# Optimization experiments

Hardware: AMD Instinct MI355X
Metric: run time of the kernel (lower is better)

Reference implementation:

```python
import jax, jax.numpy as jnp
import numpy as np

N = 50000   # nodes per side
H = 256     # hidden_dim
E = 800000  # edges per metapath (avg degree 16)
XAVIER_STD = 0.088  # gain 1.414 * sqrt(2/(H+H))


def setup_inputs() -> dict:
    key = jax.random.key(0)
    ks = jax.random.split(key, 32)
    inp = {}
    inp["h_d"] = jax.random.normal(ks[0], (N, H), dtype=jnp.float32)
    inp["h_p"] = jax.random.normal(ks[1], (N, H), dtype=jnp.float32)
    i = 2
    for name in ["d0", "d1", "p0", "p1"]:
        inp[name + "_idx"] = jax.random.randint(ks[i], (2, E), 0, N, dtype=jnp.int32); i += 1
        inp[name + "_val"] = jax.random.uniform(ks[i], (E,), dtype=jnp.float32); i += 1
    # per-metapath GCN params: Linear weight [H,H] (no bias), additive bias [H], PReLU slope (scalar)
    for name in ["d0", "d1", "p0", "p1"]:
        inp["W" + name] = jax.random.normal(ks[i], (H, H), dtype=jnp.float32) * XAVIER_STD; i += 1
        inp["b" + name] = jnp.zeros((H,), jnp.float32)
        inp["a" + name] = jnp.full((1,), 0.25, jnp.float32)
    # per-side attention params: fc weight/bias, att vector [1,H]
    for s in ["d", "p"]:
        inp["fcW" + s] = jax.random.normal(ks[i], (H, H), dtype=jnp.float32) * XAVIER_STD; i += 1
        inp["fcb" + s] = jnp.zeros((H,), jnp.float32)
        inp["att" + s] = jax.random.normal(ks[i], (1, H), dtype=jnp.float32) * XAVIER_STD; i += 1
    return inp


def _gcn(h, W, b, a, idx, val):
    # Linear (no bias) -> sparse COO spmm -> bias -> PReLU
    fts = h @ W.T                                  # [N,H]
    msg = val[:, None] * fts[idx[1]]               # gather source rows [E,H]
    out = jax.ops.segment_sum(msg, idx[0], num_segments=h.shape[0]) + b
    return jnp.where(out > 0, out, a * out)        # PReLU, shared slope


def _attn_fuse(embeds, Wf, bf, att):
    # score_p = att . mean_n(tanh(fc(embed_p)))  -> softmax over metapaths
    sp = jnp.stack([jnp.tanh(e @ Wf.T + bf).mean(axis=0) for e in embeds])  # [P,H]
    beta = jax.nn.softmax(sp @ att[0])                                      # [P]
    return jnp.einsum('p,pnh->nh', beta, jnp.stack(embeds))


def reference(h_d, h_p, d0_idx, d0_val, d1_idx, d1_val, p0_idx, p0_val,
              p1_idx, p1_val, Wd0, bd0, ad0, Wd1, bd1, ad1,
              Wp0, bp0, ap0, Wp1, bp1, ap1,
              fcWd, fcbd, attd, fcWp, fcbp, attp):
    embeds_d = [_gcn(h_d, Wd0, bd0, ad0, d0_idx, d0_val),
                _gcn(h_d, Wd1, bd1, ad1, d1_idx, d1_val)]
    z_d = _attn_fuse(embeds_d, fcWd, fcbd, attd)
    embeds_p = [_gcn(h_p, Wp0, bp0, ap0, p0_idx, p0_val),
                _gcn(h_p, Wp1, bp1, ap1, p1_idx, p1_val)]
    z_p = _attn_fuse(embeds_p, fcWp, fcbp, attp)
    return (z_d, z_p)
```

## Files before the change

kernel.cpp:

```cpp
#include <hip/hip_runtime.h>
#include <cstdint>

#define H 256
#define NBMAX 400
#define CAPB 16

typedef unsigned short u16;
typedef __attribute__((ext_vector_type(8))) short short8;
typedef __attribute__((ext_vector_type(4))) float f32x4;

__device__ __forceinline__ float bf2f(u16 u) {
  return __uint_as_float(((unsigned)u) << 16);
}
__device__ __forceinline__ u16 f2bf(float f) {
  unsigned u = __float_as_uint(f);
  u = (u + 0x7FFF + ((u >> 16) & 1)) >> 16;
  return (u16)u;
}
__device__ __forceinline__ void async16(const void* g, void* l) {
  __builtin_amdgcn_global_load_lds((const __attribute__((address_space(1))) void*)g,
                                   (__attribute__((address_space(3))) void*)l, 16, 0, 0);
}

__global__ __launch_bounds__(256) void cvt_bf16(
    const float* __restrict__ src, u16* __restrict__ dst, int total)
{
  int i = (blockIdx.x * 256 + threadIdx.x) * 4;
  if (i >= total) return;
  float4 x = *(const float4*)(src + i);
  *(ushort4*)(dst + i) = make_ushort4(f2bf(x.x), f2bf(x.y), f2bf(x.z), f2bf(x.w));
}

__global__ __launch_bounds__(256) void cvt_weights(
    const float* w0, const float* w1, const float* w2, const float* w3,
    const float* w4, const float* w5, u16* __restrict__ dst)
{
  const float* srcs[6] = {w0, w1, w2, w3, w4, w5};
  const float* s = srcs[blockIdx.y];
  int i = (blockIdx.x * 256 + threadIdx.x) * 4;
  float4 x = *(const float4*)(s + i);
  *(ushort4*)(dst + blockIdx.y * (H * H) + i) =
      make_ushort4(f2bf(x.x), f2bf(x.y), f2bf(x.z), f2bf(x.w));
}

__device__ __forceinline__ int block_incl_scan(int v) {
  __shared__ int wsum[4];
  int tid = threadIdx.x, lane = tid & 63, w = tid >> 6;
  int x = v;
  #pragma unroll
  for (int off = 1; off < 64; off <<= 1) {
    int n = __shfl_up(x, off);
    if (lane >= off) x += n;
  }
  if (lane == 63) wsum[w] = x;
  __syncthreads();
  int add = 0;
  #pragma unroll
  for (int i = 0; i < 4; ++i) add += (i < w) ? wsum[i] : 0;
  return x + add;
}

__global__ __launch_bounds__(1024) void hist_coarse(
    const int* i0, const int* i1, const int* i2, const int* i3,
    int* __restrict__ bcnt, int E, int nbuck)
{
  int mp = blockIdx.y;
  const int* idxs[4] = {i0, i1, i2, i3};
  const int* idx = idxs[mp];
  __shared__ int lh[NBMAX];
  int t = threadIdx.x;
  for (int i = t; i < nbuck; i += 1024) lh[i] = 0;
  __syncthreads();
  for (int e = blockIdx.x * 1024 + t; e < E; e += gridDim.x * 1024)
    atomicAdd(&lh[idx[e] >> 7], 1);
  __syncthreads();
  for (int i = t; i < nbuck; i += 1024) {
    int v = lh[i];
    if (v) atomicAdd(&bcnt[mp * nbuck + i], v);
  }
}

__global__ __launch_bounds__(256) void scan_buckets(
    const int* __restrict__ bcnt, int* __restrict__ bbase,
    int* __restrict__ gcur, int* __restrict__ rowptr, int N, int E, int nbuck)
{
  int mp = blockIdx.y;
  int t = threadIdx.x;
  int i0 = t * 2, i1 = t * 2 + 1;
  int a = (i0 < nbuck) ? bcnt[mp * nbuck + i0] : 0;
  int b = (i1 < nbuck) ? bcnt[mp * nbuck + i1] : 0;
  int s = a + b;
  int incl = block_incl_scan(s);
  int ex = incl - s;
  if (i0 < nbuck) { bbase[mp * nbuck + i0] = ex;     gcur[mp * nbuck + i0] = ex; }
  if (i1 < nbuck) { bbase[mp * nbuck + i1] = ex + a; gcur[mp * nbuck + i1] = ex + a; }
  if (t == 0) rowptr[mp * (N + 1) + N] = E;
}

__global__ __launch_bounds__(1024) void scatter_binned(
    const int* i0, const int* i1, const int* i2, const int* i3,
    const float* v0, const float* v1, const float* v2, const float* v3,
    int* __restrict__ gcur, int2* __restrict__ edgesB, int E, int nbuck)
{
  int mp = blockIdx.y;
  const int* idxs[4] = {i0, i1, i2, i3};
  const float* vals[4] = {v0, v1, v2, v3};
  const int* idx = idxs[mp];
  const float* val = vals[mp];
  int* cur = gcur + mp * nbuck;
  int2* out = edgesB + (size_t)mp * E;

  __shared__ int cnt[NBMAX];
  __shared__ int2 slab[NBMAX * CAPB];
  int t = threadIdx.x;
  for (int i = t; i < nbuck; i += 1024) cnt[i] = 0;
  __syncthreads();

  for (int base_e = blockIdx.x * 2048; base_e < E; base_e += gridDim.x * 2048) {
    #pragma unroll
    for (int u = 0; u < 2; ++u) {
      int e = base_e + u * 1024 + t;
      if (e < E) {
        int d = idx[e];
        int s = idx[E + e];
        float v = val[e];
        int bb = d >> 7;
        int2 pk = make_int2(s | ((d & 127) << 16), __float_as_int(v));
        int slot = atomicAdd(&cnt[bb], 1);
        if (slot < CAPB) slab[bb * CAPB + slot] = pk;
        else {
          int pos = atomicAdd(&cur[bb], 1);
          out[pos] = pk;
        }
      }
    }
    __syncthreads();
    for (int bb = t; bb < nbuck; bb += 1024) {
      int c = cnt[bb];
      if (c > CAPB) c = CAPB;
      if (c >= 8) {
        int ng = c >> 3;
        int pos = atomicAdd(&cur[bb], ng * 8);
        for (int k = 0; k < ng * 8; ++k) out[pos + k] = slab[bb * CAPB + k];
        int r = c & 7;
        for (int k = 0; k < r; ++k)
          slab[bb * CAPB + k] = slab[bb * CAPB + ng * 8 + k];
        cnt[bb] = r;
      }
    }
    __syncthreads();
  }
  for (int bb = t; bb < nbuck; bb += 1024) {
    int c = cnt[bb];
    if (c > CAPB) c = CAPB;
    if (c > 0) {
      int pos = atomicAdd(&cur[bb], c);
      for (int k = 0; k < c; ++k) out[pos + k] = slab[bb * CAPB + k];
    }
  }
}

__global__ __launch_bounds__(256) void bucket_to_csr(
    const int2* __restrict__ edgesB, const int* __restrict__ bbase,
    int* __restrict__ rowptr, int2* __restrict__ edges, int N, int E, int nbuck)
{
  int mp = blockIdx.y;
  int b = blockIdx.x;
  int base = bbase[mp * nbuck + b];
  int endp = (b + 1 < nbuck) ? bbase[mp * nbuck + b + 1] : E;
  int cntE = endp - base;
  const int2* in = edgesB + (size_t)mp * E + base;
  int2* out = edges + (size_t)mp * E;

  __shared__ int h[128], csum[128];
  int t = threadIdx.x;
  if (t < 128) h[t] = 0;
  __syncthreads();
  for (int k = t; k < cntE; k += 256)
    atomicAdd(&h[(in[k].x >> 16) & 127], 1);
  __syncthreads();
  if (t == 0) {
    int acc = 0;
    for (int i = 0; i < 128; ++i) { int c = h[i]; csum[i] = acc; acc += c; }
  }
  __syncthreads();
  int d0 = b << 7;
  if (t < 128 && d0 + t < N) rowptr[mp * (N + 1) + d0 + t] = base + csum[t];
  if (t < 128) h[t] = csum[t];
  __syncthreads();
  for (int k = t; k < cntE; k += 256) {
    int2 pk = in[k];
    int dl = (pk.x >> 16) & 127;
    int pos = atomicAdd(&h[dl], 1);
    out[base + pos] = make_int2(pk.x & 0xFFFF, pk.y);
  }
}

__global__ __launch_bounds__(256) void spmm_csr(
    const u16* __restrict__ fts, const int* __restrict__ rowptr,
    const int2* __restrict__ edges, const float* __restrict__ bias,
    const float* __restrict__ alpha, u16* __restrict__ e, int N)
{
  int gw = (int)((blockIdx.x * 256 + threadIdx.x) >> 6);
  if (gw >= N) return;
  int lane = threadIdx.x & 63;
  int beg = rowptr[gw], end = rowptr[gw + 1];
  float a0 = 0.f, a1 = 0.f, a2 = 0.f, a3 = 0.f;
  for (int base = beg; base < end; base += 64) {
    int k = base + lane;
    int2 ev = make_int2(0, 0);
    if (k < end) ev = edges[k];
    int cnt = min(64, end - base);
    int j = 0;
    for (; j + 4 <= cnt; j += 4) {
      int sj[4]; float vj[4]; ushort4 r[4];
      #pragma unroll
      for (int u = 0; u < 4; ++u) {
        sj[u] = __shfl(ev.x, j + u);
        vj[u] = __uint_as_float((unsigned)__shfl(ev.y, j + u));
      }
      #pragma unroll
      for (int u = 0; u < 4; ++u)
        r[u] = *(const ushort4*)(fts + (size_t)sj[u] * H + lane * 4);
      #pragma unroll
      for (int u = 0; u < 4; ++u) {
        a0 += vj[u] * bf2f(r[u].x);
        a1 += vj[u] * bf2f(r[u].y);
        a2 += vj[u] * bf2f(r[u].z);
        a3 += vj[u] * bf2f(r[u].w);
      }
    }
    for (; j < cnt; ++j) {
      int sj = __shfl(ev.x, j);
      float vj = __uint_as_float((unsigned)__shfl(ev.y, j));
      ushort4 r = *(const ushort4*)(fts + (size_t)sj * H + lane * 4);
      a0 += vj * bf2f(r.x);
      a1 += vj * bf2f(r.y);
      a2 += vj * bf2f(r.z);
      a3 += vj * bf2f(r.w);
    }
  }
  int c = lane * 4;
  float al = alpha[0];
  float r0 = a0 + bias[c],     r1 = a1 + bias[c + 1];
  float r2 = a2 + bias[c + 2], r3 = a3 + bias[c + 3];
  r0 = r0 > 0.f ? r0 : al * r0;
  r1 = r1 > 0.f ? r1 : al * r1;
  r2 = r2 > 0.f ? r2 : al * r2;
  r3 = r3 > 0.f ? r3 : al * r3;
  *(ushort4*)(e + (size_t)gw * H + c) =
      make_ushort4(f2bf(r0), f2bf(r1), f2bf(r2), f2bf(r3));
}

template <int MODE>
__global__ __launch_bounds__(256) void gemm_bt(
    const u16* __restrict__ A, const u16* __restrict__ W,
    u16* __restrict__ C, const float* __restrict__ bias,
    float* __restrict__ colsum, int M)
{
  __shared__ u16 As[128 * 64];
  __shared__ u16 Bs[128 * 64];
  const int tid  = threadIdx.x;
  const int lane = tid & 63;
  const int wave = tid >> 6;
  const int quad = lane >> 4;
  const int l15  = lane & 15;
  const int m0 = blockIdx.x * 128;
  const int n0 = blockIdx.y * 128;
  const int wr = (wave & 1) * 64;
  const int wc = (wave >> 1) * 64;

  f32x4 acc[4][4] = {};

  for (int k0 = 0; k0 < H; k0 += 64) {
    #pragma unroll
    for (int r = 0; r < 4; ++r) {
      int chunk = r * 256 + tid;
      int row = chunk >> 3;
      int col = (chunk & 7) * 8;
      int gm = m0 + row; if (gm >= M) gm = M - 1;
      u16* lbase = As + (r * 256 + wave * 64) * 8;
      async16(A + gm * H + k0 + col, lbase);
      u16* lbase2 = Bs + (r * 256 + wave * 64) * 8;
      async16(W + (n0 + row) * H + k0 + col, lbase2);
    }
    __syncthreads();
    #pragma unroll
    for (int kk = 0; kk < 64; kk += 32) {
      short8 af[4], bf[4];
      #pragma unroll
      for (int i = 0; i < 4; ++i) {
        af[i] = *(const short8*)(As + (wr + i * 16 + l15) * 64 + kk + quad * 8);
        bf[i] = *(const short8*)(Bs + (wc + i * 16 + l15) * 64 + kk + quad * 8);
      }
      #pragma unroll
      for (int mi = 0; mi < 4; ++mi)
        #pragma unroll
        for (int ni = 0; ni < 4; ++ni)
          acc[mi][ni] = __builtin_amdgcn_mfma_f32_16x16x32_bf16(af[mi], bf[ni], acc[mi][ni], 0, 0, 0);
    }
    __syncthreads();
  }

  if (MODE == 0) {
    #pragma unroll
    for (int mi = 0; mi < 4; ++mi)
      #pragma unroll
      for (int ni = 0; ni < 4; ++ni) {
        int n = n0 + wc + ni * 16 + l15;
        #pragma unroll
        for (int j = 0; j < 4; ++j) {
          int m = m0 + wr + mi * 16 + quad * 4 + j;
          if (m < M) C[m * H + n] = f2bf(acc[mi][ni][j]);
        }
      }
  } else {
    #pragma unroll
    for (int ni = 0; ni < 4; ++ni) {
      int n = n0 + wc + ni * 16 + l15;
      float bv = bias[n];
      float s = 0.f;
      #pragma unroll
      for (int mi = 0; mi < 4; ++mi)
        #pragma unroll
        for (int j = 0; j < 4; ++j) {
          int m = m0 + wr + mi * 16 + quad * 4 + j;
          if (m < M) {
            float x = acc[mi][ni][j] + bv;
            s += 1.f - 2.f / (__expf(2.f * x) + 1.f);
          }
        }
      s += __shfl_xor(s, 16);
      s += __shfl_xor(s, 32);
      if (lane < 16) unsafeAtomicAdd(&colsum[n], s);
    }
  }
}

__global__ __launch_bounds__(256) void compute_beta(
    const float* __restrict__ sp, const float* __restrict__ att,
    float invN, float* __restrict__ beta)
{
  __shared__ float red0[4], red1[4];
  int t = threadIdx.x;
  float a = att[t];
  float s0 = sp[t] * invN * a;
  float s1 = sp[H + t] * invN * a;
  #pragma unroll
  for (int off = 32; off > 0; off >>= 1) {
    s0 += __shfl_down(s0, off);
    s1 += __shfl_down(s1, off);
  }
  int lane = t & 63, w = t >> 6;
  if (lane == 0) { red0[w] = s0; red1[w] = s1; }
  __syncthreads();
  if (t == 0) {
    float a0 = red0[0] + red0[1] + red0[2] + red0[3];
    float a1 = red1[0] + red1[1] + red1[2] + red1[3];
    float mx = fmaxf(a0, a1);
    float e0v = __expf(a0 - mx), e1v = __expf(a1 - mx);
    float inv = 1.f / (e0v + e1v);
    beta[0] = e0v * inv;
    beta[1] = e1v * inv;
  }
}

__global__ __launch_bounds__(256) void fuse_out(
    const u16* __restrict__ e0, const u16* __restrict__ e1,
    const float* __restrict__ beta, float* __restrict__ out, int total)
{
  int i = (blockIdx.x * 256 + threadIdx.x) * 4;
  if (i >= total) return;
  float b0 = beta[0], b1 = beta[1];
  ushort4 u0 = *(const ushort4*)(e0 + i);
  ushort4 u1 = *(const ushort4*)(e1 + i);
  float4 o;
  o.x = b0 * bf2f(u0.x) + b1 * bf2f(u1.x);
  o.y = b0 * bf2f(u0.y) + b1 * bf2f(u1.y);
  o.z = b0 * bf2f(u0.z) + b1 * bf2f(u1.z);
  o.w = b0 * bf2f(u0.w) + b1 * bf2f(u1.w);
  *(float4*)(out + i) = o;
}

extern "C" void kernel_launch(void* const* d_in, const int* in_sizes, int n_in,
                              void* d_out, int out_size, void* d_ws, size_t ws_size,
                              hipStream_t stream)
{
  const float* h_in[2] = {(const float*)d_in[0], (const float*)d_in[1]};
  const int N = in_sizes[0] / H;
  const int E = in_sizes[3];
  const int* idx[4]; const float* val[4];
  for (int i = 0; i < 4; ++i) {
    idx[i] = (const int*)d_in[2 + 2 * i];
    val[i] = (const float*)d_in[3 + 2 * i];
  }
  const float *W[4], *bia[4], *alp[4];
  for (int i = 0; i < 4; ++i) {
    W[i]   = (const float*)d_in[10 + 3 * i];
    bia[i] = (const float*)d_in[11 + 3 * i];
    alp[i] = (const float*)d_in[12 + 3 * i];
  }
  const float *fcW[2], *fcb[2], *att[2];
  for (int s = 0; s < 2; ++s) {
    fcW[s] = (const float*)d_in[22 + 3 * s];
    fcb[s] = (const float*)d_in[23 + 3 * s];
    att[s] = (const float*)d_in[24 + 3 * s];
  }

  const size_t NH = (size_t)N * H;
  const int nbuck = (N + 127) >> 7;
  auto align256 = [](size_t x) { return (x + 255) & ~(size_t)255; };
  char* p = (char*)d_ws;
  u16* fts = (u16*)p;      p += align256(NH * 2);
  u16* e0b = (u16*)p;      p += align256(NH * 2);
  u16* hbf = (u16*)p;      p += align256(NH * 2);
  u16* Wbf = (u16*)p;      p += align256((size_t)6 * H * H * 2);
  int* bcnt = (int*)p;     p += align256((size_t)4 * NBMAX * 4);
  int* bbase = (int*)p;    p += align256((size_t)4 * NBMAX * 4);
  int* gcur = (int*)p;     p += align256((size_t)4 * NBMAX * 4);
  int* rowptr = (int*)p;   p += align256((size_t)4 * (N + 1) * 4);
  int2* edges = (int2*)p;  p += align256((size_t)4 * E * 8);
  float* sp = (float*)p;   p += align256((size_t)2 * H * 4);
  float* beta = (float*)p;
  u16* e1b = hbf;
  int2* edgesB = (int2*)fts;

  const int gx = (N + 127) / 128;
  dim3 ggrid(gx, 2);
  const int tot = (int)NH;
  const int el_blocks = tot / 4 / 256;
  const int spmm_blocks = (N + 3) / 4;

  dim3 wgrid(H * H / 1024, 6);
  cvt_weights<<<wgrid, 256, 0, stream>>>(W[0], W[1], W[2], W[3], fcW[0], fcW[1], Wbf);

  hipMemsetAsync(bcnt, 0, (size_t)4 * NBMAX * 4, stream);
  hist_coarse<<<dim3(64, 4), 1024, 0, stream>>>(idx[0], idx[1], idx[2], idx[3],
                                                bcnt, E, nbuck);
  scan_buckets<<<dim3(1, 4), 256, 0, stream>>>(bcnt, bbase, gcur, rowptr, N, E, nbuck);
  scatter_binned<<<dim3(64, 4), 1024, 0, stream>>>(idx[0], idx[1], idx[2], idx[3],
                                                   val[0], val[1], val[2], val[3],
                                                   gcur, edgesB, E, nbuck);
  bucket_to_csr<<<dim3(nbuck, 4), 256, 0, stream>>>(edgesB, bbase, rowptr, edges,
                                                    N, E, nbuck);

  for (int s = 0; s < 2; ++s) {
    float* outz = (float*)d_out + (size_t)s * NH;
    cvt_bf16<<<el_blocks, 256, 0, stream>>>(h_in[s], hbf, tot);

    for (int m = 0; m < 2; ++m) {
      int pi = s * 2 + m;
      gemm_bt<0><<<ggrid, 256, 0, stream>>>(hbf, Wbf + (size_t)pi * H * H, fts,
                                            nullptr, nullptr, N);
      spmm_csr<<<spmm_blocks, 256, 0, stream>>>(
          fts, rowptr + (size_t)pi * (N + 1), edges + (size_t)pi * E,
          bia[pi], alp[pi], m == 0 ? e0b : e1b, N);
    }
    hipMemsetAsync(sp, 0, 2 * H * 4, stream);
    gemm_bt<1><<<ggrid, 256, 0, stream>>>(e0b, Wbf + (size_t)(4 + s) * H * H,
                                          nullptr, fcb[s], sp, N);
    gemm_bt<1><<<ggrid, 256, 0, stream>>>(e1b, Wbf + (size_t)(4 + s) * H * H,
                                          nullptr, fcb[s], sp + H, N);
    compute_beta<<<1, 256, 0, stream>>>(sp, att[s], 1.0f / (float)N, beta);
    fuse_out<<<el_blocks, 256, 0, stream>>>(e0b, e1b, beta, outz, tot);
  }
}
```

Before: 808.4 us.

## Batch all four metapaths into single grid-dimension launches per stage

Replaces the per-side, per-metapath loop of many small launches with one launch per stage (convert, projection GEMM, SpMM, attention GEMM, beta, fuse), each indexing its metapath or side through an extra grid dimension. This cuts launch count and serialization gaps and gives each launch more blocks to fill the GPU. In exchange the workspace grows to hold all four feature and embedding buffers at once, which raises memory footprint and may reduce L2 reuse. Index arithmetic is widened to size_t to handle the larger buffers.

```diff
diff --git a/kernel.cpp b/kernel.cpp
--- a/kernel.cpp
+++ b/kernel.cpp
@@ -23,12 +23,15 @@
 }
 
 __global__ __launch_bounds__(256) void cvt_bf16(
-    const float* __restrict__ src, u16* __restrict__ dst, int total)
-{
+    const float* __restrict__ h0, const float* __restrict__ h1,
+    u16* __restrict__ dst, int total, size_t NH)
+{
+  const float* src = blockIdx.y ? h1 : h0;
+  u16* d = dst + (size_t)blockIdx.y * NH;
   int i = (blockIdx.x * 256 + threadIdx.x) * 4;
   if (i >= total) return;
   float4 x = *(const float4*)(src + i);
-  *(ushort4*)(dst + i) = make_ushort4(f2bf(x.x), f2bf(x.y), f2bf(x.z), f2bf(x.w));
+  *(ushort4*)(d + i) = make_ushort4(f2bf(x.x), f2bf(x.y), f2bf(x.z), f2bf(x.w));
 }
 
 __global__ __launch_bounds__(256) void cvt_weights(
@@ -197,10 +200,22 @@
 }
 
 __global__ __launch_bounds__(256) void spmm_csr(
-    const u16* __restrict__ fts, const int* __restrict__ rowptr,
-    const int2* __restrict__ edges, const float* __restrict__ bias,
-    const float* __restrict__ alpha, u16* __restrict__ e, int N)
-{
+    const u16* __restrict__ ftsAll, const int* __restrict__ rowptrAll,
+    const int2* __restrict__ edgesAll,
+    const float* b0, const float* b1, const float* b2, const float* b3,
+    const float* a0ptr, const float* a1ptr, const float* a2ptr, const float* a3ptr,
+    u16* __restrict__ eAll, int N, int E, size_t NH)
+{
+  int mp = blockIdx.y;
+  const u16* fts = ftsAll + (size_t)mp * NH;
+  const int* rowptr = rowptrAll + (size_t)mp * (N + 1);
+  const int2* edges = edgesAll + (size_t)mp * E;
+  const float* biases[4] = {b0, b1, b2, b3};
+  const float* alphas[4] = {a0ptr, a1ptr, a2ptr, a3ptr};
+  const float* bias = biases[mp];
+  const float* alpha = alphas[mp];
+  u16* e = eAll + (size_t)mp * NH;
+
   int gw = (int)((blockIdx.x * 256 + threadIdx.x) >> 6);
   if (gw >= N) return;
   int lane = threadIdx.x & 63;
@@ -254,10 +269,24 @@
 
 template <int MODE>
 __global__ __launch_bounds__(256) void gemm_bt(
-    const u16* __restrict__ A, const u16* __restrict__ W,
-    u16* __restrict__ C, const float* __restrict__ bias,
-    float* __restrict__ colsum, int M)
-{
+    const u16* __restrict__ Abase, const u16* __restrict__ Wbase,
+    u16* __restrict__ Cbase, const float* fcb0, const float* fcb1,
+    float* __restrict__ colsum, int M, size_t NH)
+{
+  const int pi = blockIdx.z;
+  const u16* A; const u16* W; u16* C = nullptr;
+  const float* bias = nullptr; float* cs = nullptr;
+  if (MODE == 0) {
+    A = Abase + (size_t)(pi >> 1) * NH;
+    W = Wbase + (size_t)pi * (H * H);
+    C = Cbase + (size_t)pi * NH;
+  } else {
+    A = Abase + (size_t)pi * NH;
+    W = Wbase + (size_t)(pi >> 1) * (H * H);
+    bias = (pi >> 1) ? fcb1 : fcb0;
+    cs = colsum + (size_t)pi * H;
+  }
+
   __shared__ u16 As[128 * 64];
   __shared__ u16 Bs[128 * 64];
   const int tid  = threadIdx.x;
@@ -280,9 +309,9 @@
       int col = (chunk & 7) * 8;
       int gm = m0 + row; if (gm >= M) gm = M - 1;
       u16* lbase = As + (r * 256 + wave * 64) * 8;
-      async16(A + gm * H + k0 + col, lbase);
+      async16(A + (size_t)gm * H + k0 + col, lbase);
       u16* lbase2 = Bs + (r * 256 + wave * 64) * 8;
-      async16(W + (n0 + row) * H + k0 + col, lbase2);
+      async16(W + (size_t)(n0 + row) * H + k0 + col, lbase2);
     }
     __syncthreads();
     #pragma unroll
@@ -311,7 +340,7 @@
         #pragma unroll
         for (int j = 0; j < 4; ++j) {
           int m = m0 + wr + mi * 16 + quad * 4 + j;
-          if (m < M) C[m * H + n] = f2bf(acc[mi][ni][j]);
+          if (m < M) C[(size_t)m * H + n] = f2bf(acc[mi][ni][j]);
         }
       }
   } else {
@@ -332,20 +361,23 @@
         }
       s += __shfl_xor(s, 16);
       s += __shfl_xor(s, 32);
-      if (lane < 16) unsafeAtomicAdd(&colsum[n], s);
+      if (lane < 16) unsafeAtomicAdd(&cs[n], s);
     }
   }
 }
 
 __global__ __launch_bounds__(256) void compute_beta(
-    const float* __restrict__ sp, const float* __restrict__ att,
+    const float* __restrict__ sp, const float* attd, const float* attp,
     float invN, float* __restrict__ beta)
 {
   __shared__ float red0[4], red1[4];
+  int s = blockIdx.y;
+  const float* att = s ? attp : attd;
+  const float* spb = sp + (size_t)(2 * s) * H;
   int t = threadIdx.x;
   float a = att[t];
-  float s0 = sp[t] * invN * a;
-  float s1 = sp[H + t] * invN * a;
+  float s0 = spb[t] * invN * a;
+  float s1 = spb[H + t] * invN * a;
   #pragma unroll
   for (int off = 32; off > 0; off >>= 1) {
     s0 += __shfl_down(s0, off);
@@ -360,26 +392,30 @@
     float mx = fmaxf(a0, a1);
     float e0v = __expf(a0 - mx), e1v = __expf(a1 - mx);
     float inv = 1.f / (e0v + e1v);
-    beta[0] = e0v * inv;
-    beta[1] = e1v * inv;
+    beta[2 * s]     = e0v * inv;
+    beta[2 * s + 1] = e1v * inv;
   }
 }
 
 __global__ __launch_bounds__(256) void fuse_out(
-    const u16* __restrict__ e0, const u16* __restrict__ e1,
-    const float* __restrict__ beta, float* __restrict__ out, int total)
-{
+    const u16* __restrict__ eAll, const float* __restrict__ beta,
+    float* __restrict__ out, int total, size_t NH)
+{
+  int s = blockIdx.y;
+  const u16* e0 = eAll + (size_t)(2 * s) * NH;
+  const u16* e1 = eAll + (size_t)(2 * s + 1) * NH;
+  float* o = out + (size_t)s * NH;
   int i = (blockIdx.x * 256 + threadIdx.x) * 4;
   if (i >= total) return;
-  float b0 = beta[0], b1 = beta[1];
+  float b0 = beta[2 * s], b1 = beta[2 * s + 1];
   ushort4 u0 = *(const ushort4*)(e0 + i);
   ushort4 u1 = *(const ushort4*)(e1 + i);
-  float4 o;
-  o.x = b0 * bf2f(u0.x) + b1 * bf2f(u1.x);
-  o.y = b0 * bf2f(u0.y) + b1 * bf2f(u1.y);
-  o.z = b0 * bf2f(u0.z) + b1 * bf2f(u1.z);
-  o.w = b0 * bf2f(u0.w) + b1 * bf2f(u1.w);
-  *(float4*)(out + i) = o;
+  float4 ov;
+  ov.x = b0 * bf2f(u0.x) + b1 * bf2f(u1.x);
+  ov.y = b0 * bf2f(u0.y) + b1 * bf2f(u1.y);
+  ov.z = b0 * bf2f(u0.z) + b1 * bf2f(u1.z);
+  ov.w = b0 * bf2f(u0.w) + b1 * bf2f(u1.w);
+  *(float4*)(o + i) = ov;
 }
 
 extern "C" void kernel_launch(void* const* d_in, const int* in_sizes, int n_in,
@@ -411,30 +447,29 @@
   const int nbuck = (N + 127) >> 7;
   auto align256 = [](size_t x) { return (x + 255) & ~(size_t)255; };
   char* p = (char*)d_ws;
-  u16* fts = (u16*)p;      p += align256(NH * 2);
-  u16* e0b = (u16*)p;      p += align256(NH * 2);
-  u16* hbf = (u16*)p;      p += align256(NH * 2);
+  u16* hbf = (u16*)p;      p += align256((size_t)2 * NH * 2);
+  u16* fts = (u16*)p;      p += align256((size_t)4 * NH * 2);
+  u16* eAll = (u16*)p;     p += align256((size_t)4 * NH * 2);
   u16* Wbf = (u16*)p;      p += align256((size_t)6 * H * H * 2);
   int* bcnt = (int*)p;     p += align256((size_t)4 * NBMAX * 4);
   int* bbase = (int*)p;    p += align256((size_t)4 * NBMAX * 4);
   int* gcur = (int*)p;     p += align256((size_t)4 * NBMAX * 4);
   int* rowptr = (int*)p;   p += align256((size_t)4 * (N + 1) * 4);
   int2* edges = (int2*)p;  p += align256((size_t)4 * E * 8);
-  float* sp = (float*)p;   p += align256((size_t)2 * H * 4);
+  float* sp = (float*)p;   p += align256((size_t)4 * H * 4);
   float* beta = (float*)p;
-  u16* e1b = hbf;
   int2* edgesB = (int2*)fts;
 
   const int gx = (N + 127) / 128;
-  dim3 ggrid(gx, 2);
   const int tot = (int)NH;
-  const int el_blocks = tot / 4 / 256;
+  const int el_blocks = (tot / 4 + 255) / 256;
   const int spmm_blocks = (N + 3) / 4;
 
   dim3 wgrid(H * H / 1024, 6);
   cvt_weights<<<wgrid, 256, 0, stream>>>(W[0], W[1], W[2], W[3], fcW[0], fcW[1], Wbf);
 
   hipMemsetAsync(bcnt, 0, (size_t)4 * NBMAX * 4, stream);
+  hipMemsetAsync(sp, 0, (size_t)4 * H * 4, stream);
   hist_coarse<<<dim3(64, 4), 1024, 0, stream>>>(idx[0], idx[1], idx[2], idx[3],
                                                 bcnt, E, nbuck);
   scan_buckets<<<dim3(1, 4), 256, 0, stream>>>(bcnt, bbase, gcur, rowptr, N, E, nbuck);
@@ -444,24 +479,22 @@
   bucket_to_csr<<<dim3(nbuck, 4), 256, 0, stream>>>(edgesB, bbase, rowptr, edges,
                                                     N, E, nbuck);
 
-  for (int s = 0; s < 2; ++s) {
-    float* outz = (float*)d_out + (size_t)s * NH;
-    cvt_bf16<<<el_blocks, 256, 0, stream>>>(h_in[s], hbf, tot);
-
-    for (int m = 0; m < 2; ++m) {
-      int pi = s * 2 + m;
-      gemm_bt<0><<<ggrid, 256, 0, stream>>>(hbf, Wbf + (size_t)pi * H * H, fts,
-                                            nullptr, nullptr, N);
-      spmm_csr<<<spmm_blocks, 256, 0, stream>>>(
-          fts, rowptr + (size_t)pi * (N + 1), edges + (size_t)pi * E,
-          bia[pi], alp[pi], m == 0 ? e0b : e1b, N);
-    }
-    hipMemsetAsync(sp, 0, 2 * H * 4, stream);
-    gemm_bt<1><<<ggrid, 256, 0, stream>>>(e0b, Wbf + (size_t)(4 + s) * H * H,
-                                          nullptr, fcb[s], sp, N);
-    gemm_bt<1><<<ggrid, 256, 0, stream>>>(e1b, Wbf + (size_t)(4 + s) * H * H,
-                                          nullptr, fcb[s], sp + H, N);
-    compute_beta<<<1, 256, 0, stream>>>(sp, att[s], 1.0f / (float)N, beta);
-    fuse_out<<<el_blocks, 256, 0, stream>>>(e0b, e1b, beta, outz, tot);
-  }
-}
+  cvt_bf16<<<dim3(el_blocks, 2), 256, 0, stream>>>(h_in[0], h_in[1], hbf, tot, NH);
+
+  gemm_bt<0><<<dim3(gx, 2, 4), 256, 0, stream>>>(hbf, Wbf, fts,
+                                                 nullptr, nullptr, nullptr, N, NH);
+
+  spmm_csr<<<dim3(spmm_blocks, 4), 256, 0, stream>>>(
+      fts, rowptr, edges,
+      bia[0], bia[1], bia[2], bia[3],
+      alp[0], alp[1], alp[2], alp[3],
+      eAll, N, E, NH);
+
+  gemm_bt<1><<<dim3(gx, 2, 4), 256, 0, stream>>>(eAll, Wbf + (size_t)4 * H * H,
+                                                 nullptr, fcb[0], fcb[1], sp, N, NH);
+
+  compute_beta<<<dim3(1, 2), 256, 0, stream>>>(sp, att[0], att[1],
+                                               1.0f / (float)N, beta);
+
+  fuse_out<<<dim3(el_blocks, 2), 256, 0, stream>>>(eAll, beta, (float*)d_out, tot, NH);
+}
```

Result: faster. 689.8 us (-14.7%).
